# Performance work log

Hardware: AMD Instinct MI355X
Metric: run time of the kernel (lower is better)

The kernel has to match this reference:

```python
import jax, jax.numpy as jnp
import numpy as np
import math

DIM = 1024
N_HEADS = 16
HEAD_DIM = DIM // N_HEADS


def rope(x):
    # x: [B, H, S, D] with D == HEAD_DIM, interleaved even/odd rotation
    S = x.shape[-2]
    D = x.shape[-1]
    pos = jnp.arange(S, dtype=x.dtype)[:, None]              # [S, 1]
    dim = jnp.arange(D // 2, dtype=x.dtype)[None, :]         # [1, D/2]
    theta = pos / jnp.exp(2.0 * dim / D * math.log(10000.0))  # [S, D/2]
    sin = jnp.sin(theta)[None, None]                          # [1,1,S,D/2]
    cos = jnp.cos(theta)[None, None]
    x1 = x[..., ::2]
    x2 = x[..., 1::2]
    out1 = x1 * cos - x2 * sin
    out2 = x1 * sin + x2 * cos
    # interleave back: stack on last axis then flatten pairs
    return jnp.stack([out1, out2], axis=-1).reshape(x.shape)


def setup_inputs() -> dict:
    key = jax.random.key(0)
    ks = jax.random.split(key, 9)
    B, S = 2, 2048
    s = 1.0 / math.sqrt(DIM)
    inp = {
        "x": jax.random.normal(ks[0], (B, S, DIM), dtype=jnp.float32),
        "wq": jax.random.normal(ks[1], (DIM, DIM), dtype=jnp.float32) * s,
        "bq": jnp.zeros((DIM,), dtype=jnp.float32),
        "wk": jax.random.normal(ks[2], (DIM, DIM), dtype=jnp.float32) * s,
        "bk": jnp.zeros((DIM,), dtype=jnp.float32),
        "wv": jax.random.normal(ks[3], (DIM, DIM), dtype=jnp.float32) * s,
        "bv": jnp.zeros((DIM,), dtype=jnp.float32),
        "wo": jax.random.normal(ks[4], (DIM, DIM), dtype=jnp.float32) * s,
        "bo": jnp.zeros((DIM,), dtype=jnp.float32),
    }
    return inp


def reference(x, wq, bq, wk, bk, wv, bv, wo, bo):
    B, S, _ = x.shape
    # torch Linear: y = x @ W^T + b
    def proj(w, b):
        y = jnp.einsum('bsd,ed->bse', x, w) + b
        return y.reshape(B, S, N_HEADS, HEAD_DIM).transpose(0, 2, 1, 3)  # [B,H,S,Dh]
    q = rope(proj(wq, bq))
    k = rope(proj(wk, bk))
    v = proj(wv, bv)
    score = jnp.einsum('bhqd,bhkd->bhqk', q, k) / math.sqrt(HEAD_DIM)
    causal = jnp.tril(jnp.ones((S, S), dtype=bool))
    score = jnp.where(causal[None, None], score, -jnp.inf)
    attn = jax.nn.softmax(score, axis=-1)
    out = jnp.einsum('bhqk,bhkd->bhqd', attn, v)
    out = out.transpose(0, 2, 1, 3).reshape(B, S, DIM)
    return jnp.einsum('bsd,ed->bse', out, wo) + bo
```

## Files before the change

### kernel.cpp

```cpp
#include <hip/hip_runtime.h>
#include <cstdint>
#include <cstddef>
#include <cmath>


typedef __bf16 bf16_t;
typedef __bf16 bf16x8 __attribute__((ext_vector_type(8)));
typedef __bf16 bf16x4 __attribute__((ext_vector_type(4)));
typedef float  f32x4  __attribute__((ext_vector_type(4)));

#define DEVFN __device__ __forceinline__

static constexpr int Bn  = 2;
static constexpr int S   = 2048;
static constexpr int DIM = 1024;
static constexpr int NH  = 16;
static constexpr int HD  = 64;
static constexpr int Mrows = Bn * S;

DEVFN f32x4 mfma16(bf16x8 a, bf16x8 b, f32x4 c) {
  return __builtin_amdgcn_mfma_f32_16x16x32_bf16(a, b, c, 0, 0, 0);
}

DEVFN void gl_lds16(const bf16_t* g, bf16_t* l) {
  __builtin_amdgcn_global_load_lds(
      (const __attribute__((address_space(1))) unsigned*)g,
      (__attribute__((address_space(3))) unsigned*)l, 16, 0, 0);
}

DEVFN float fast_exp2(float x) { return exp2f(x); }

__global__ __launch_bounds__(256) void k_prep(
    const float* __restrict__ x, const float* __restrict__ wq,
    const float* __restrict__ wk, const float* __restrict__ wv,
    const float* __restrict__ wo, bf16_t* __restrict__ xb,
    bf16_t* __restrict__ wqb, bf16_t* __restrict__ wkb,
    bf16_t* __restrict__ wvb, bf16_t* __restrict__ wob,
    float2* __restrict__ tab) {
  const int bid = blockIdx.x;
  if (bid < 8192) {
    const float* src;
    bf16_t* dst;
    size_t base;
    if (bid < 4096) {
      src = x; dst = xb; base = (size_t)bid << 10;
    } else {
      int wsel = (bid - 4096) >> 10;
      src = wsel == 0 ? wq : wsel == 1 ? wk : wsel == 2 ? wv : wo;
      dst = wsel == 0 ? wqb : wsel == 1 ? wkb : wsel == 2 ? wvb : wob;
      base = (size_t)((bid - 4096) & 1023) << 10;
    }
    size_t i = base + (size_t)threadIdx.x * 4;
    float4 v = *(const float4*)(src + i);
    bf16x4 o = { (bf16_t)v.x, (bf16_t)v.y, (bf16_t)v.z, (bf16_t)v.w };
    *(bf16x4*)(dst + i) = o;
  } else {
    int i = (bid - 8192) * 256 + threadIdx.x;
    int s = i >> 5, d = i & 31;
    float th = (float)s * expf((float)d * -0.2878231366f);
    tab[i] = make_float2(cosf(th), sinf(th));
  }
}

__global__ __launch_bounds__(256) void k_rope(bf16_t* __restrict__ X,
                                              const float2* __restrict__ tab,
                                              float scale) {
  int i = blockIdx.x * 256 + threadIdx.x;
  int row = i >> 7;
  int s = row & (S - 1);
  int dd = (i & 7) << 3;
  int p0 = dd >> 1;
  bf16x8 v = *(bf16x8*)(X + (size_t)i * 8);
  bf16x8 o;
#pragma unroll
  for (int j = 0; j < 4; ++j) {
    float x1 = (float)v[2 * j], x2 = (float)v[2 * j + 1];
    float2 cs = tab[s * 32 + p0 + j];
    o[2 * j]     = (bf16_t)((x1 * cs.x - x2 * cs.y) * scale);
    o[2 * j + 1] = (bf16_t)((x1 * cs.y + x2 * cs.x) * scale);
  }
  *(bf16x8*)(X + (size_t)i * 8) = o;
}

__global__ __launch_bounds__(256) void k_trans(const bf16_t* __restrict__ Vin,
                                               bf16_t* __restrict__ VT) {
  __shared__ __align__(16) bf16_t tile[64][72];
  int s0 = blockIdx.x * 64, bh = blockIdx.y;
  int b = bh >> 4, h = bh & 15;
  int t = threadIdx.x;
#pragma unroll
  for (int it = 0; it < 2; ++it) {
    int sl = (t >> 3) + it * 32, d0 = (t & 7) << 3;
    *(bf16x8*)&tile[sl][d0] =
        *(const bf16x8*)(Vin + (size_t)(b * S + s0 + sl) * DIM + h * HD + d0);
  }
  __syncthreads();
  int d = t >> 2, c0 = (t & 3) * 16;
  bf16_t buf[16];
#pragma unroll
  for (int j = 0; j < 16; ++j) buf[j] = tile[c0 + j][d];
  bf16_t* op = VT + ((size_t)bh * HD + d) * S + s0 + c0;
  *(bf16x8*)op = *(bf16x8*)&buf[0];
  *(bf16x8*)(op + 8) = *(bf16x8*)&buf[8];
}

DEVFN void stage64(const bf16_t* __restrict__ A, const bf16_t* __restrict__ Bw,
                   bf16_t* Al, bf16_t* Bl, int m0, int n0, int k0, int t,
                   int w) {
#pragma unroll
  for (int ld = 0; ld < 4; ++ld) {
    int c = t + ld * 256;
    int row = c >> 3;
    int j = ((c & 7) ^ (row & 7)) << 3;
    bf16_t* dstA = Al + (size_t)(w * 64 + ld * 256) * 8;
    bf16_t* dstB = Bl + (size_t)(w * 64 + ld * 256) * 8;
    gl_lds16(A + (size_t)(m0 + row) * DIM + k0 + j, dstA);
    gl_lds16(Bw + (size_t)(n0 + row) * DIM + k0 + j, dstB);
  }
}

__global__ __launch_bounds__(256) void k_gemm_qkv(
    const bf16_t* __restrict__ A, const bf16_t* __restrict__ Wall,
    const float* __restrict__ c0, const float* __restrict__ c1,
    const float* __restrict__ c2, bf16_t* __restrict__ Oq,
    bf16_t* __restrict__ Ok, bf16_t* __restrict__ Ov_) {
  __shared__ __align__(16) bf16_t Al[128 * 64];
  __shared__ __align__(16) bf16_t Bl[128 * 64];
  const int t = threadIdx.x, w = t >> 6, l = t & 63;
  const int lr = l & 15, lc = l >> 4;
  const int lid = blockIdx.x;
  const int xcd = lid & 7, s = lid >> 3;
  const int my = ((xcd >> 1) << 3) + (s & 7);
  const int nx = (xcd & 1) * 12 + (s >> 3);
  const int m0 = my * 128, n0g = nx * 128;
  const int z = n0g >> 10, n0l = n0g & 1023;
  const int wr = w >> 1, wc = w & 1;
  f32x4 acc[4][4] = {};

  for (int k0 = 0; k0 < DIM; k0 += 64) {
    __syncthreads();
    stage64(A, Wall, Al, Bl, m0, n0g, k0, t, w);
    asm volatile("s_waitcnt vmcnt(0)" ::: "memory");
    __syncthreads();
    bf16x8 af[2][4], bfr[2][4];
#pragma unroll
    for (int ks = 0; ks < 2; ++ks) {
#pragma unroll
      for (int mi = 0; mi < 4; ++mi) {
        int row = wr * 64 + mi * 16 + lr;
        int off = ((ks * 4 + lc) << 4) ^ ((row & 7) << 4);
        af[ks][mi] = *(const bf16x8*)((const char*)Al + row * 128 + off);
      }
#pragma unroll
      for (int ni = 0; ni < 4; ++ni) {
        int row = wc * 64 + ni * 16 + lr;
        int off = ((ks * 4 + lc) << 4) ^ ((row & 7) << 4);
        bfr[ks][ni] = *(const bf16x8*)((const char*)Bl + row * 128 + off);
      }
    }
    __builtin_amdgcn_s_setprio(1);
#pragma unroll
    for (int ks = 0; ks < 2; ++ks)
#pragma unroll
      for (int mi = 0; mi < 4; ++mi)
#pragma unroll
        for (int ni = 0; ni < 4; ++ni)
          acc[mi][ni] = mfma16(af[ks][mi], bfr[ks][ni], acc[mi][ni]);
    __builtin_amdgcn_s_setprio(0);
  }

  bf16_t* Ov = z == 0 ? Oq : (z == 1 ? Ok : Ov_);
  const float* bias = z == 0 ? c0 : (z == 1 ? c1 : c2);
#pragma unroll
  for (int ni = 0; ni < 4; ++ni) {
    const int col = n0l + wc * 64 + ni * 16 + lr;
    const float bv = bias[col];
#pragma unroll
    for (int mi = 0; mi < 4; ++mi)
#pragma unroll
      for (int r = 0; r < 4; ++r) {
        int row = m0 + wr * 64 + mi * 16 + lc * 4 + r;
        Ov[(size_t)row * DIM + col] = (bf16_t)(acc[mi][ni][r] + bv);
      }
  }
}

__global__ __launch_bounds__(256) void k_gemm_out(
    const bf16_t* __restrict__ A, const bf16_t* __restrict__ Bw,
    const float* __restrict__ bias, float* __restrict__ Ov) {
  __shared__ __align__(16) bf16_t Al[128 * 64];
  __shared__ __align__(16) bf16_t Bl[128 * 64];
  const int t = threadIdx.x, w = t >> 6, l = t & 63;
  const int lr = l & 15, lc = l >> 4;
  const int lid = blockIdx.x;
  const int xcd = lid & 7, s = lid >> 3;
  const int my = ((xcd >> 1) << 3) + (s & 7);
  const int nx = (xcd & 1) * 4 + (s >> 3);
  const int m0 = my * 128, n0 = nx * 128;
  const int wr = w >> 1, wc = w & 1;
  f32x4 acc[4][4] = {};

  for (int k0 = 0; k0 < DIM; k0 += 64) {
    __syncthreads();
    stage64(A, Bw, Al, Bl, m0, n0, k0, t, w);
    asm volatile("s_waitcnt vmcnt(0)" ::: "memory");
    __syncthreads();
    bf16x8 af[2][4], bfr[2][4];
#pragma unroll
    for (int ks = 0; ks < 2; ++ks) {
#pragma unroll
      for (int mi = 0; mi < 4; ++mi) {
        int row = wr * 64 + mi * 16 + lr;
        int off = ((ks * 4 + lc) << 4) ^ ((row & 7) << 4);
        af[ks][mi] = *(const bf16x8*)((const char*)Al + row * 128 + off);
      }
#pragma unroll
      for (int ni = 0; ni < 4; ++ni) {
        int row = wc * 64 + ni * 16 + lr;
        int off = ((ks * 4 + lc) << 4) ^ ((row & 7) << 4);
        bfr[ks][ni] = *(const bf16x8*)((const char*)Bl + row * 128 + off);
      }
    }
    __builtin_amdgcn_s_setprio(1);
#pragma unroll
    for (int ks = 0; ks < 2; ++ks)
#pragma unroll
      for (int mi = 0; mi < 4; ++mi)
#pragma unroll
        for (int ni = 0; ni < 4; ++ni)
          acc[mi][ni] = mfma16(af[ks][mi], bfr[ks][ni], acc[mi][ni]);
    __builtin_amdgcn_s_setprio(0);
  }

#pragma unroll
  for (int ni = 0; ni < 4; ++ni) {
    int col = n0 + wc * 64 + ni * 16 + lr;
    float bv = bias[col];
#pragma unroll
    for (int mi = 0; mi < 4; ++mi)
#pragma unroll
      for (int r = 0; r < 4; ++r) {
        int row = m0 + wr * 64 + mi * 16 + lc * 4 + r;
        Ov[(size_t)row * DIM + col] = acc[mi][ni][r] + bv;
      }
  }
}

DEVFN void stage_kv(const bf16_t* __restrict__ Kc,
                    const bf16_t* __restrict__ VT, bf16_t* Kb, bf16_t* Vb,
                    int b, int bh, int h, int k0, int tid, int w) {
#pragma unroll
  for (int ld = 0; ld < 2; ++ld) {
    int c = tid + ld * 256;
    int row = c >> 3;
    int j = ((c & 7) ^ (row & 7)) << 3;
    bf16_t* dstK = Kb + (size_t)(w * 64 + ld * 256) * 8;
    bf16_t* dstV = Vb + (size_t)(w * 64 + ld * 256) * 8;
    gl_lds16(Kc + (size_t)(b * S + k0 + row) * DIM + h * HD + j, dstK);
    gl_lds16(VT + ((size_t)bh * HD + row) * S + k0 + j, dstV);
  }
}

__global__ __launch_bounds__(256) void k_attn(const bf16_t* __restrict__ Q,
                                              const bf16_t* __restrict__ Kc,
                                              const bf16_t* __restrict__ VT,
                                              bf16_t* __restrict__ O) {
  __shared__ __align__(16) bf16_t Kl[2][64 * 64];
  __shared__ __align__(16) bf16_t Vl[2][64 * 64];
  __shared__ __align__(16) bf16_t Pl[4][16 * 64];
  const int tid = threadIdx.x, w = tid >> 6, l = tid & 63;
  const int lr = l & 15, lc = l >> 4;
  const int lid = blockIdx.x + (blockIdx.y << 4);
  const int xcd = lid & 7, slot = lid >> 3;
  const int bh = xcd * 4 + (slot >> 4);
  const int a = slot & 15;
  const int b = bh >> 4, h = bh & 15;
  char* Pw = (char*)&Pl[w][0];

#pragma unroll 1
  for (int pi = 0; pi < 2; ++pi) {
    const int tile = (pi == 0) ? a : 31 - a;
    const int q0 = tile * 64;
    const int nt = tile + 1;

    bf16x8 qf[2];
    {
      const bf16_t* qp =
          Q + (size_t)(b * S + q0 + w * 16 + lr) * DIM + h * HD + lc * 8;
      qf[0] = *(const bf16x8*)qp;
      qf[1] = *(const bf16x8*)(qp + 32);
    }
    f32x4 o[4] = {};
    float m_run = -INFINITY;
    float rowsum = 0.f;

    stage_kv(Kc, VT, &Kl[0][0], &Vl[0][0], b, bh, h, 0, tid, w);

#pragma unroll 1
    for (int it = 0; it < nt; ++it) {
      const int cur = it & 1;
      const bf16_t* Kb = &Kl[cur][0];
      const bf16_t* Vb = &Vl[cur][0];
      if (it + 1 < nt) {
        stage_kv(Kc, VT, &Kl[cur ^ 1][0], &Vl[cur ^ 1][0], b, bh, h,
                 (it + 1) * 64, tid, w);
        asm volatile("s_waitcnt vmcnt(4)" ::: "memory");
      } else {
        asm volatile("s_waitcnt vmcnt(0)" ::: "memory");
      }
      __builtin_amdgcn_s_barrier();
      __builtin_amdgcn_sched_barrier(0);

      f32x4 s[4] = {};
      __builtin_amdgcn_s_setprio(1);
#pragma unroll
      for (int ks = 0; ks < 2; ++ks) {
#pragma unroll
        for (int ni = 0; ni < 4; ++ni) {
          int row = ni * 16 + lr;
          int off = (ks * 64 + lc * 16) ^ ((row & 7) << 4);
          bf16x8 kf = *(const bf16x8*)((const char*)Kb + row * 128 + off);
          s[ni] = mfma16(kf, qf[ks], s[ni]);
        }
      }
      __builtin_amdgcn_s_setprio(0);

      if (it == tile) {
        const int qloc = w * 16 + lr;
#pragma unroll
        for (int ni = 0; ni < 4; ++ni)
#pragma unroll
          for (int r = 0; r < 4; ++r)
            if (ni * 16 + lc * 4 + r > qloc) s[ni][r] = -INFINITY;
      }

      float m01 = fmaxf(fmaxf(s[0][0], s[0][1]), fmaxf(s[0][2], s[0][3]));
      float m23 = fmaxf(fmaxf(s[1][0], s[1][1]), fmaxf(s[1][2], s[1][3]));
      float m45 = fmaxf(fmaxf(s[2][0], s[2][1]), fmaxf(s[2][2], s[2][3]));
      float m67 = fmaxf(fmaxf(s[3][0], s[3][1]), fmaxf(s[3][2], s[3][3]));
      float pm = fmaxf(fmaxf(m01, m23), fmaxf(m45, m67));
      pm = fmaxf(pm, __shfl_xor(pm, 16));
      pm = fmaxf(pm, __shfl_xor(pm, 32));

      if (__ballot(pm > m_run + 8.f)) {
        float mn = fmaxf(m_run, pm);
        float alpha = fast_exp2(m_run - mn);
        m_run = mn;
        rowsum *= alpha;
#pragma unroll
        for (int r = 0; r < 4; ++r) {
          float aq = __shfl(alpha, lc * 4 + r);
#pragma unroll
          for (int ni = 0; ni < 4; ++ni) o[ni][r] *= aq;
        }
      }

      float rs = 0.f;
#pragma unroll
      for (int ni = 0; ni < 4; ++ni) {
        float p0 = fast_exp2(s[ni][0] - m_run);
        float p1 = fast_exp2(s[ni][1] - m_run);
        float p2 = fast_exp2(s[ni][2] - m_run);
        float p3 = fast_exp2(s[ni][3] - m_run);
        rs += (p0 + p1) + (p2 + p3);
        bf16x4 pb = { (bf16_t)p0, (bf16_t)p1, (bf16_t)p2, (bf16_t)p3 };
        *(bf16x4*)(Pw + (lr * 128 + ((ni * 32 + lc * 8) ^ ((lr & 7) << 4)))) =
            pb;
      }
      rs += __shfl_xor(rs, 16);
      rs += __shfl_xor(rs, 32);
      rowsum += rs;

      __builtin_amdgcn_s_setprio(1);
#pragma unroll
      for (int ks = 0; ks < 2; ++ks) {
        int off = ks * 64 + lc * 16;
        bf16x8 pa =
            *(const bf16x8*)(Pw + lr * 128 + (off ^ ((lr & 7) << 4)));
#pragma unroll
        for (int ni = 0; ni < 4; ++ni) {
          int vrow = ni * 16 + lr;
          bf16x8 vb = *(const bf16x8*)((const char*)Vb + vrow * 128 +
                                       (off ^ ((vrow & 7) << 4)));
          o[ni] = mfma16(pa, vb, o[ni]);
        }
      }
      __builtin_amdgcn_s_setprio(0);

      __builtin_amdgcn_s_barrier();
    }

    float inv[4];
#pragma unroll
    for (int r = 0; r < 4; ++r) inv[r] = 1.0f / __shfl(rowsum, lc * 4 + r);
#pragma unroll
    for (int ni = 0; ni < 4; ++ni)
#pragma unroll
      for (int r = 0; r < 4; ++r) {
        int qr = q0 + w * 16 + lc * 4 + r;
        float v = o[ni][r] * inv[r];
        O[(size_t)(b * S + qr) * DIM + h * HD + ni * 16 + lr] = (bf16_t)v;
      }
  }
}

extern "C" void kernel_launch(void* const* d_in, const int* in_sizes, int n_in,
                              void* d_out, int out_size, void* d_ws,
                              size_t ws_size, hipStream_t stream) {
  const float* x  = (const float*)d_in[0];
  const float* wq = (const float*)d_in[1];
  const float* bq = (const float*)d_in[2];
  const float* wk = (const float*)d_in[3];
  const float* bk = (const float*)d_in[4];
  const float* wv = (const float*)d_in[5];
  const float* bv = (const float*)d_in[6];
  const float* wo = (const float*)d_in[7];
  const float* bo = (const float*)d_in[8];

  const size_t MD = (size_t)Mrows * DIM;
  const size_t WD = (size_t)DIM * DIM;
  bf16_t* W = (bf16_t*)d_ws;
  bf16_t* x_bf  = W;
  bf16_t* wq_bf = x_bf + MD;
  bf16_t* wk_bf = wq_bf + WD;
  bf16_t* wv_bf = wk_bf + WD;
  bf16_t* wo_bf = wv_bf + WD;
  bf16_t* q_lin = wo_bf + WD;
  bf16_t* k_lin = q_lin + MD;
  bf16_t* v_lin = k_lin + MD;
  bf16_t* vT    = v_lin + MD;
  float2* tab   = (float2*)(vT + MD);
  bf16_t* attn_out = x_bf;

  k_prep<<<8448, 256, 0, stream>>>(x, wq, wk, wv, wo, x_bf, wq_bf, wk_bf,
                                   wv_bf, wo_bf, tab);

  k_gemm_qkv<<<768, 256, 0, stream>>>(x_bf, wq_bf, bq, bk, bv, q_lin, k_lin,
                                      v_lin);

  k_rope<<<2048, 256, 0, stream>>>(q_lin, tab, 0.125f * 1.4426950408889634f);
  k_rope<<<2048, 256, 0, stream>>>(k_lin, tab, 1.0f);
  k_trans<<<dim3(S / 64, Bn * NH), 256, 0, stream>>>(v_lin, vT);

  k_attn<<<dim3(16, Bn * NH), 256, 0, stream>>>(q_lin, k_lin, vT, attn_out);

  k_gemm_out<<<256, 256, 0, stream>>>(attn_out, wo_bf, bo, (float*)d_out);
}
```

Before: 134.3 us.

## Double attention KV tile width to 128 keys per iteration

The attention kernel now processes 128 keys per inner iteration instead of 64. The K/V staging, LDS buffers, P scratch, softmax reductions and causal mask are resized to match, which halves the number of barriers and loop iterations per query tile. The cost is roughly double the LDS footprint and more live score registers. On the diagonal block the kernel also computes and masks some keys that lie entirely beyond the causal boundary, which adds wasted MFMA work.

After: 132.3 us. No clear change (-1.5%).

```diff
diff --git a/kernel.cpp b/kernel.cpp
--- a/kernel.cpp
+++ b/kernel.cpp
@@ -250,14 +250,16 @@
                     const bf16_t* __restrict__ VT, bf16_t* Kb, bf16_t* Vb,
                     int b, int bh, int h, int k0, int tid, int w) {
 #pragma unroll
-  for (int ld = 0; ld < 2; ++ld) {
+  for (int ld = 0; ld < 4; ++ld) {
     int c = tid + ld * 256;
-    int row = c >> 3;
-    int j = ((c & 7) ^ (row & 7)) << 3;
     bf16_t* dstK = Kb + (size_t)(w * 64 + ld * 256) * 8;
     bf16_t* dstV = Vb + (size_t)(w * 64 + ld * 256) * 8;
-    gl_lds16(Kc + (size_t)(b * S + k0 + row) * DIM + h * HD + j, dstK);
-    gl_lds16(VT + ((size_t)bh * HD + row) * S + k0 + j, dstV);
+    int krow = c >> 3;
+    int kj = ((c & 7) ^ (krow & 7)) << 3;
+    gl_lds16(Kc + (size_t)(b * S + k0 + krow) * DIM + h * HD + kj, dstK);
+    int vrow = c >> 4;
+    int vj = ((c & 15) ^ (vrow & 7)) << 3;
+    gl_lds16(VT + ((size_t)bh * HD + vrow) * S + k0 + vj, dstV);
   }
 }
 
@@ -265,9 +267,9 @@
                                               const bf16_t* __restrict__ Kc,
                                               const bf16_t* __restrict__ VT,
                                               bf16_t* __restrict__ O) {
-  __shared__ __align__(16) bf16_t Kl[2][64 * 64];
-  __shared__ __align__(16) bf16_t Vl[2][64 * 64];
-  __shared__ __align__(16) bf16_t Pl[4][16 * 64];
+  __shared__ __align__(16) bf16_t Kl[2][128 * 64];
+  __shared__ __align__(16) bf16_t Vl[2][64 * 128];
+  __shared__ __align__(16) bf16_t Pl[4][16 * 128];
   const int tid = threadIdx.x, w = tid >> 6, l = tid & 63;
   const int lr = l & 15, lc = l >> 4;
   const int lid = blockIdx.x + (blockIdx.y << 4);
@@ -281,7 +283,7 @@
   for (int pi = 0; pi < 2; ++pi) {
     const int tile = (pi == 0) ? a : 31 - a;
     const int q0 = tile * 64;
-    const int nt = tile + 1;
+    const int nt = (tile >> 1) + 1;
 
     bf16x8 qf[2];
     {
@@ -303,20 +305,22 @@
       const bf16_t* Vb = &Vl[cur][0];
       if (it + 1 < nt) {
         stage_kv(Kc, VT, &Kl[cur ^ 1][0], &Vl[cur ^ 1][0], b, bh, h,
-                 (it + 1) * 64, tid, w);
-        asm volatile("s_waitcnt vmcnt(4)" ::: "memory");
+                 (it + 1) * 128, tid, w);
+        asm volatile("s_waitcnt vmcnt(8)" ::: "memory");
       } else {
         asm volatile("s_waitcnt vmcnt(0)" ::: "memory");
       }
       __builtin_amdgcn_s_barrier();
       __builtin_amdgcn_sched_barrier(0);
 
-      f32x4 s[4] = {};
+      f32x4 s[8];
+#pragma unroll
+      for (int ni = 0; ni < 8; ++ni) s[ni] = f32x4{0.f, 0.f, 0.f, 0.f};
       __builtin_amdgcn_s_setprio(1);
 #pragma unroll
       for (int ks = 0; ks < 2; ++ks) {
 #pragma unroll
-        for (int ni = 0; ni < 4; ++ni) {
+        for (int ni = 0; ni < 8; ++ni) {
           int row = ni * 16 + lr;
           int off = (ks * 64 + lc * 16) ^ ((row & 7) << 4);
           bf16x8 kf = *(const bf16x8*)((const char*)Kb + row * 128 + off);
@@ -325,20 +329,21 @@
       }
       __builtin_amdgcn_s_setprio(0);
 
-      if (it == tile) {
-        const int qloc = w * 16 + lr;
-#pragma unroll
-        for (int ni = 0; ni < 4; ++ni)
+      if (it == nt - 1) {
+        const int qloc = q0 - (nt - 1) * 128 + w * 16 + lr;
+#pragma unroll
+        for (int ni = 0; ni < 8; ++ni)
 #pragma unroll
           for (int r = 0; r < 4; ++r)
             if (ni * 16 + lc * 4 + r > qloc) s[ni][r] = -INFINITY;
       }
 
-      float m01 = fmaxf(fmaxf(s[0][0], s[0][1]), fmaxf(s[0][2], s[0][3]));
-      float m23 = fmaxf(fmaxf(s[1][0], s[1][1]), fmaxf(s[1][2], s[1][3]));
-      float m45 = fmaxf(fmaxf(s[2][0], s[2][1]), fmaxf(s[2][2], s[2][3]));
-      float m67 = fmaxf(fmaxf(s[3][0], s[3][1]), fmaxf(s[3][2], s[3][3]));
-      float pm = fmaxf(fmaxf(m01, m23), fmaxf(m45, m67));
+      float mm[8];
+#pragma unroll
+      for (int ni = 0; ni < 8; ++ni)
+        mm[ni] = fmaxf(fmaxf(s[ni][0], s[ni][1]), fmaxf(s[ni][2], s[ni][3]));
+      float pm = fmaxf(fmaxf(fmaxf(mm[0], mm[1]), fmaxf(mm[2], mm[3])),
+                       fmaxf(fmaxf(mm[4], mm[5]), fmaxf(mm[6], mm[7])));
       pm = fmaxf(pm, __shfl_xor(pm, 16));
       pm = fmaxf(pm, __shfl_xor(pm, 32));
 
@@ -357,14 +362,14 @@
 
       float rs = 0.f;
 #pragma unroll
-      for (int ni = 0; ni < 4; ++ni) {
+      for (int ni = 0; ni < 8; ++ni) {
         float p0 = fast_exp2(s[ni][0] - m_run);
         float p1 = fast_exp2(s[ni][1] - m_run);
         float p2 = fast_exp2(s[ni][2] - m_run);
         float p3 = fast_exp2(s[ni][3] - m_run);
         rs += (p0 + p1) + (p2 + p3);
         bf16x4 pb = { (bf16_t)p0, (bf16_t)p1, (bf16_t)p2, (bf16_t)p3 };
-        *(bf16x4*)(Pw + (lr * 128 + ((ni * 32 + lc * 8) ^ ((lr & 7) << 4)))) =
+        *(bf16x4*)(Pw + (lr * 256 + ((ni * 32 + lc * 8) ^ ((lr & 7) << 4)))) =
             pb;
       }
       rs += __shfl_xor(rs, 16);
@@ -373,14 +378,14 @@
 
       __builtin_amdgcn_s_setprio(1);
 #pragma unroll
-      for (int ks = 0; ks < 2; ++ks) {
+      for (int ks = 0; ks < 4; ++ks) {
         int off = ks * 64 + lc * 16;
         bf16x8 pa =
-            *(const bf16x8*)(Pw + lr * 128 + (off ^ ((lr & 7) << 4)));
+            *(const bf16x8*)(Pw + lr * 256 + (off ^ ((lr & 7) << 4)));
 #pragma unroll
         for (int ni = 0; ni < 4; ++ni) {
           int vrow = ni * 16 + lr;
-          bf16x8 vb = *(const bf16x8*)((const char*)Vb + vrow * 128 +
+          bf16x8 vb = *(const bf16x8*)((const char*)Vb + vrow * 256 +
                                        (off ^ ((vrow & 7) << 4)));
           o[ni] = mfma16(pa, vb, o[ni]);
         }
```
